# Kernel optimization log

Hardware: AMD Instinct MI355X
Metric: run time of the kernel (lower is better)

## Reference

```python
import jax, jax.numpy as jnp
import numpy as np

N = 4096          # number of leaves
M = 2 * N - 1     # total tree nodes
B = 256           # batch of distribution pairs


def setup_inputs() -> dict:
    key = jax.random.key(0)
    k0, k1, k2, k3, k4, k5 = jax.random.split(key, 6)
    # ancestor-indicator matrix: mostly zeros (structured sparse used densely)
    subtree = (jax.random.uniform(k0, (M, N)) < 0.01).astype(jnp.float32)
    d1 = jax.random.uniform(k1, (N, B), dtype=jnp.float32)
    d2 = jax.random.uniform(k2, (N, B), dtype=jnp.float32)
    ot_distances = jax.random.uniform(k3, (B,), dtype=jnp.float32)
    param = jax.random.normal(k4, (M,), dtype=jnp.float32)
    parents = jax.random.randint(k5, (M,), 0, M, dtype=jnp.int32)
    return {"d1": d1, "d2": d2, "ot_distances": ot_distances,
            "subtree": subtree, "param": param, "parents": parents}


def reference(d1, d2, ot_distances, subtree, param, parents):
    # aggregate leaf mass to every tree node: [M, B]
    m_d1 = jnp.matmul(subtree, d1)
    m_d2 = jnp.matmul(subtree, d2)
    # edge weight = parent height - node height: [M]
    w_v = param[parents] - param
    # tree-Wasserstein-1 per pair: [B]
    w1_tree = 0.5 * jnp.matmul(w_v, jnp.abs(m_d1 - m_d2))
    return jnp.sum(jnp.square(ot_distances - w1_tree))
```

## Files before the change

### kernel.cpp

```cpp
#include <hip/hip_runtime.h>

#define NN    4096
#define MM    8191
#define BB    256
#define HCAP  128

typedef float nfloat4 __attribute__((ext_vector_type(4)));

__device__ __forceinline__ int prefix_lt(unsigned long long m) {
    return __builtin_amdgcn_mbcnt_hi((unsigned)(m >> 32),
           __builtin_amdgcn_mbcnt_lo((unsigned)m, 0u));
}

__device__ __forceinline__ unsigned pack2bf(float lo, float hi) {
    unsigned a = __float_as_uint(lo);
    unsigned b = __float_as_uint(hi);
    a += 0x7fffu + ((a >> 16) & 1u);
    b += 0x7fffu + ((b >> 16) & 1u);
    return (a >> 16) | (b & 0xffff0000u);
}

__global__ __launch_bounds__(256) void k_prep(const float4* __restrict__ d1,
                                              const float4* __restrict__ d2,
                                              float* __restrict__ part2,
                                              uint2* __restrict__ ddp) {
    int idx = blockIdx.x * 256 + threadIdx.x;
    if (idx < 256 * BB) part2[idx] = 0.0f;
    float4 a = d1[idx], b = d2[idx];
    uint2 r;
    r.x = pack2bf(a.x - b.x, a.y - b.y);
    r.y = pack2bf(a.z - b.z, a.w - b.w);
    ddp[idx] = r;
}

__global__ __launch_bounds__(256, 4) void k_fused(
        const nfloat4* __restrict__ st4,
        const uint2* __restrict__ ddp,
        const float* __restrict__ param,
        const int*   __restrict__ parents,
        float* __restrict__ part2) {
    __shared__ unsigned short s_list[2][2][2][HCAP];
    __shared__ int s_cnt[2][2][2];
    __shared__ int s_flag[2][2];
    __shared__ float s_part[BB];
    const int tid  = threadIdx.x;
    const int wave = tid >> 6;
    const int lane = tid & 63;

    s_part[tid] = 0.0f;
    if (tid < 4) s_flag[tid >> 1][tid & 1] = 0;
    __syncthreads();

    const int pipe = wave & 1;
    const int base = blockIdx.x * 2 + pipe;
    float q0 = 0.f, q1 = 0.f, q2 = 0.f, q3 = 0.f;

    if (wave < 2) {
        nfloat4 a0, a1, a2, a3, a4, a5, a6, a7;
        nfloat4 b0, b1, b2, b3, b4, b5, b6, b7;

        #define ISSUE(P, m, h)                                                   \
        {                                                                        \
            const nfloat4* gbase = st4 + (size_t)(m) * (NN / 4) + (h) * (NN / 8);\
            P##0 = __builtin_nontemporal_load(gbase + lane);                     \
            P##1 = __builtin_nontemporal_load(gbase + 64  + lane);               \
            P##2 = __builtin_nontemporal_load(gbase + 128 + lane);               \
            P##3 = __builtin_nontemporal_load(gbase + 192 + lane);               \
            P##4 = __builtin_nontemporal_load(gbase + 256 + lane);               \
            P##5 = __builtin_nontemporal_load(gbase + 320 + lane);               \
            P##6 = __builtin_nontemporal_load(gbase + 384 + lane);               \
            P##7 = __builtin_nontemporal_load(gbase + 448 + lane);               \
        }
        #define SITE(val, col)                                                   \
        {                                                                        \
            unsigned long long mk = __ballot((val) != 0.0f);                     \
            if ((val) != 0.0f)                                                   \
                buf[c + prefix_lt(mk)] = (unsigned short)(col);                  \
            c += __popcll(mk);                                                   \
        }
        #define QUAD(v, cb0)                                                     \
            SITE(v.x, (cb0))     SITE(v.y, (cb0) + 1)                            \
            SITE(v.z, (cb0) + 2) SITE(v.w, (cb0) + 3)
        #define COMPACT(P, h)                                                    \
        {                                                                        \
            const int cb = (h) * (NN / 2);                                       \
            QUAD(P##0, cb + (lane)       * 4)                                    \
            QUAD(P##1, cb + (64  + lane) * 4)                                    \
            QUAD(P##2, cb + (128 + lane) * 4)                                    \
            QUAD(P##3, cb + (192 + lane) * 4)                                    \
            QUAD(P##4, cb + (256 + lane) * 4)                                    \
            QUAD(P##5, cb + (320 + lane) * 4)                                    \
            QUAD(P##6, cb + (384 + lane) * 4)                                    \
            QUAD(P##7, cb + (448 + lane) * 4)                                    \
        }

        if (base < MM) ISSUE(a, base, 0);
        #pragma unroll 1
        for (int i = 0; i < 4; ++i) {
            const int m = base + i * 2048;
            if (m >= MM) break;
            const int slot = i & 1;
            ISSUE(b, m, 1);

            volatile int* f = &s_flag[pipe][slot];
            while (*f != 0) __builtin_amdgcn_s_sleep(2);
            __threadfence_block();

            unsigned short* buf;
            int c;
            buf = s_list[pipe][slot][0]; c = 0;
            COMPACT(a, 0);
            if (lane == 0) s_cnt[pipe][slot][0] = c;

            const int mn = base + (i + 1) * 2048;
            if (mn < MM) ISSUE(a, mn, 0);

            buf = s_list[pipe][slot][1]; c = 0;
            COMPACT(b, 1);
            if (lane == 0) s_cnt[pipe][slot][1] = c;

            __threadfence_block();
            if (lane == 0) *f = i + 1;
        }
        #undef COMPACT
        #undef QUAD
        #undef SITE
        #undef ISSUE
    } else {
        #define UNP0(u) __uint_as_float((u) << 16)
        #define UNP1(u) __uint_as_float((u) & 0xffff0000u)
        #define ACCA(g) { c0 += UNP0(g.x); c1 += UNP1(g.x); c2 += UNP0(g.y); c3 += UNP1(g.y); }
        #define ACCB(g) { e0 += UNP0(g.x); e1 += UNP1(g.x); e2 += UNP0(g.y); e3 += UNP1(g.y); }
        #pragma unroll 1
        for (int i = 0; i < 4; ++i) {
            const int m = base + i * 2048;
            if (m >= MM) break;
            const int slot = i & 1;
            volatile int* f = &s_flag[pipe][slot];
            while (*f != i + 1) __builtin_amdgcn_s_sleep(2);
            __threadfence_block();

            float c0 = 0.f, c1 = 0.f, c2 = 0.f, c3 = 0.f;
            float e0 = 0.f, e1 = 0.f, e2 = 0.f, e3 = 0.f;
            #pragma unroll
            for (int h = 0; h < 2; ++h) {
                const int c = s_cnt[pipe][slot][h];
                const unsigned short* bufr = s_list[pipe][slot][h];
                const unsigned* lw = (const unsigned*)bufr;
                int j = 0;
                for (; j + 8 <= c; j += 8) {
                    unsigned w0 = lw[(j >> 1)    ];
                    unsigned w1 = lw[(j >> 1) + 1];
                    unsigned w2 = lw[(j >> 1) + 2];
                    unsigned w3 = lw[(j >> 1) + 3];
                    unsigned o0 = (w0 & 0xffffu) * 64u + lane;
                    unsigned o1 = (w0 >> 16)     * 64u + lane;
                    unsigned o2 = (w1 & 0xffffu) * 64u + lane;
                    unsigned o3 = (w1 >> 16)     * 64u + lane;
                    unsigned o4 = (w2 & 0xffffu) * 64u + lane;
                    unsigned o5 = (w2 >> 16)     * 64u + lane;
                    unsigned o6 = (w3 & 0xffffu) * 64u + lane;
                    unsigned o7 = (w3 >> 16)     * 64u + lane;
                    uint2 g0 = ddp[o0]; uint2 g1 = ddp[o1];
                    uint2 g2 = ddp[o2]; uint2 g3 = ddp[o3];
                    uint2 g4 = ddp[o4]; uint2 g5 = ddp[o5];
                    uint2 g6 = ddp[o6]; uint2 g7 = ddp[o7];
                    ACCA(g0) ACCB(g1) ACCA(g2) ACCB(g3)
                    ACCA(g4) ACCB(g5) ACCA(g6) ACCB(g7)
                }
                for (; j + 4 <= c; j += 4) {
                    unsigned w0 = lw[(j >> 1)    ];
                    unsigned w1 = lw[(j >> 1) + 1];
                    unsigned o0 = (w0 & 0xffffu) * 64u + lane;
                    unsigned o1 = (w0 >> 16)     * 64u + lane;
                    unsigned o2 = (w1 & 0xffffu) * 64u + lane;
                    unsigned o3 = (w1 >> 16)     * 64u + lane;
                    uint2 g0 = ddp[o0]; uint2 g1 = ddp[o1];
                    uint2 g2 = ddp[o2]; uint2 g3 = ddp[o3];
                    ACCA(g0) ACCB(g1) ACCA(g2) ACCB(g3)
                }
                for (; j < c; ++j) {
                    unsigned n = bufr[j];
                    uint2 g = ddp[n * 64u + lane];
                    ACCA(g)
                }
            }
            __threadfence_block();
            if (lane == 0) *f = 0;

            const float wgt = param[parents[m]] - param[m];
            q0 += wgt * fabsf(c0 + e0);
            q1 += wgt * fabsf(c1 + e1);
            q2 += wgt * fabsf(c2 + e2);
            q3 += wgt * fabsf(c3 + e3);
        }
        #undef ACCA
        #undef ACCB
        #undef UNP0
        #undef UNP1
    }

    atomicAdd(&s_part[4 * lane + 0], q0);
    atomicAdd(&s_part[4 * lane + 1], q1);
    atomicAdd(&s_part[4 * lane + 2], q2);
    atomicAdd(&s_part[4 * lane + 3], q3);
    __syncthreads();
    atomicAdd(&part2[(size_t)(blockIdx.x & 255) * BB + tid], s_part[tid]);
}

__global__ __launch_bounds__(1024) void k_finalize(const float* __restrict__ part2,
                                                   const float* __restrict__ ot,
                                                   float* __restrict__ out) {
    __shared__ float s_red[4][BB];
    __shared__ float s_sq[16];
    const int tid = threadIdx.x;
    const int s = tid >> 8, b = tid & 255;

    float a0 = 0.f, a1 = 0.f, a2 = 0.f, a3 = 0.f;
    float a4 = 0.f, a5 = 0.f, a6 = 0.f, a7 = 0.f;
    #pragma unroll
    for (int j = 0; j < 64; j += 8) {
        int row = s * 64 + j;
        a0 += part2[(row    ) * BB + b];
        a1 += part2[(row + 1) * BB + b];
        a2 += part2[(row + 2) * BB + b];
        a3 += part2[(row + 3) * BB + b];
        a4 += part2[(row + 4) * BB + b];
        a5 += part2[(row + 5) * BB + b];
        a6 += part2[(row + 6) * BB + b];
        a7 += part2[(row + 7) * BB + b];
    }
    s_red[s][b] = ((a0 + a1) + (a2 + a3)) + ((a4 + a5) + (a6 + a7));
    __syncthreads();

    float v = 0.0f;
    if (s == 0) {
        float w1 = (s_red[0][b] + s_red[1][b]) + (s_red[2][b] + s_red[3][b]);
        float e = ot[b] - 0.5f * w1;
        v = e * e;
    }
    #pragma unroll
    for (int off = 32; off > 0; off >>= 1) v += __shfl_down(v, off, 64);
    if ((tid & 63) == 0) s_sq[tid >> 6] = v;
    __syncthreads();
    if (tid == 0) out[0] = (s_sq[0] + s_sq[1]) + (s_sq[2] + s_sq[3]);
}

extern "C" void kernel_launch(void* const* d_in, const int* in_sizes, int n_in,
                              void* d_out, int out_size, void* d_ws, size_t ws_size,
                              hipStream_t stream) {
    const float* d1      = (const float*)d_in[0];
    const float* d2      = (const float*)d_in[1];
    const float* ot      = (const float*)d_in[2];
    const float* subtree = (const float*)d_in[3];
    const float* param   = (const float*)d_in[4];
    const int*   parents = (const int*)d_in[5];

    char* wsb = (char*)d_ws;
    float* part2 = (float*)wsb;
    uint2* ddp   = (uint2*)(wsb + 256 * BB * 4);

    k_prep<<<1024, 256, 0, stream>>>((const float4*)d1, (const float4*)d2,
                                     part2, ddp);
    k_fused<<<1024, 256, 0, stream>>>((const nfloat4*)subtree, ddp,
                                      param, parents, part2);
    k_finalize<<<1, 1024, 0, stream>>>(part2, ot, (float*)d_out);
}
```

Baseline: 51.93 us.

## Widen fused kernel to four producer/consumer pipes per block, dropping register double-buffering

Blocks grow to 512 threads, so each block runs four producer/consumer wave pairs and each pipe handles two rows instead of four. The producer no longer prefetches the next half-row into a second register set; it loads and compacts one half at a time. The intent is to cut register pressure and raise occupancy (launch bounds 512,8), relying on more resident waves rather than in-wave prefetch to hide memory latency. The risk is exposed load latency per wave and a heavier block-level reduction.

```diff
diff --git a/kernel.cpp b/kernel.cpp
--- a/kernel.cpp
+++ b/kernel.cpp
@@ -33,43 +33,41 @@
     ddp[idx] = r;
 }
 
-__global__ __launch_bounds__(256, 4) void k_fused(
+__global__ __launch_bounds__(512, 8) void k_fused(
         const nfloat4* __restrict__ st4,
         const uint2* __restrict__ ddp,
         const float* __restrict__ param,
         const int*   __restrict__ parents,
         float* __restrict__ part2) {
-    __shared__ unsigned short s_list[2][2][2][HCAP];
-    __shared__ int s_cnt[2][2][2];
-    __shared__ int s_flag[2][2];
+    __shared__ unsigned short s_list[4][2][2][HCAP];
+    __shared__ int s_cnt[4][2][2];
+    __shared__ int s_flag[4][2];
     __shared__ float s_part[BB];
     const int tid  = threadIdx.x;
     const int wave = tid >> 6;
     const int lane = tid & 63;
 
-    s_part[tid] = 0.0f;
-    if (tid < 4) s_flag[tid >> 1][tid & 1] = 0;
-    __syncthreads();
-
-    const int pipe = wave & 1;
-    const int base = blockIdx.x * 2 + pipe;
+    if (tid < BB) s_part[tid] = 0.0f;
+    if (tid < 8) s_flag[tid >> 1][tid & 1] = 0;
+    __syncthreads();
+
+    const int pipe = wave & 3;
+    const int pg   = blockIdx.x * 4 + pipe;
     float q0 = 0.f, q1 = 0.f, q2 = 0.f, q3 = 0.f;
 
-    if (wave < 2) {
+    if (wave < 4) {
         nfloat4 a0, a1, a2, a3, a4, a5, a6, a7;
-        nfloat4 b0, b1, b2, b3, b4, b5, b6, b7;
-
-        #define ISSUE(P, m, h)                                                   \
+        #define ISSUE(m, h)                                                      \
         {                                                                        \
-            const nfloat4* gbase = st4 + (size_t)(m) * (NN / 4) + (h) * (NN / 8);\
-            P##0 = __builtin_nontemporal_load(gbase + lane);                     \
-            P##1 = __builtin_nontemporal_load(gbase + 64  + lane);               \
-            P##2 = __builtin_nontemporal_load(gbase + 128 + lane);               \
-            P##3 = __builtin_nontemporal_load(gbase + 192 + lane);               \
-            P##4 = __builtin_nontemporal_load(gbase + 256 + lane);               \
-            P##5 = __builtin_nontemporal_load(gbase + 320 + lane);               \
-            P##6 = __builtin_nontemporal_load(gbase + 384 + lane);               \
-            P##7 = __builtin_nontemporal_load(gbase + 448 + lane);               \
+            const nfloat4* gb = st4 + (size_t)(m) * (NN / 4) + (h) * (NN / 8);   \
+            a0 = __builtin_nontemporal_load(gb + lane);                          \
+            a1 = __builtin_nontemporal_load(gb + 64  + lane);                    \
+            a2 = __builtin_nontemporal_load(gb + 128 + lane);                    \
+            a3 = __builtin_nontemporal_load(gb + 192 + lane);                    \
+            a4 = __builtin_nontemporal_load(gb + 256 + lane);                    \
+            a5 = __builtin_nontemporal_load(gb + 320 + lane);                    \
+            a6 = __builtin_nontemporal_load(gb + 384 + lane);                    \
+            a7 = __builtin_nontemporal_load(gb + 448 + lane);                    \
         }
         #define SITE(val, col)                                                   \
         {                                                                        \
@@ -81,46 +79,42 @@
         #define QUAD(v, cb0)                                                     \
             SITE(v.x, (cb0))     SITE(v.y, (cb0) + 1)                            \
             SITE(v.z, (cb0) + 2) SITE(v.w, (cb0) + 3)
-        #define COMPACT(P, h)                                                    \
+        #define COMPACT(h)                                                       \
         {                                                                        \
             const int cb = (h) * (NN / 2);                                       \
-            QUAD(P##0, cb + (lane)       * 4)                                    \
-            QUAD(P##1, cb + (64  + lane) * 4)                                    \
-            QUAD(P##2, cb + (128 + lane) * 4)                                    \
-            QUAD(P##3, cb + (192 + lane) * 4)                                    \
-            QUAD(P##4, cb + (256 + lane) * 4)                                    \
-            QUAD(P##5, cb + (320 + lane) * 4)                                    \
-            QUAD(P##6, cb + (384 + lane) * 4)                                    \
-            QUAD(P##7, cb + (448 + lane) * 4)                                    \
-        }
-
-        if (base < MM) ISSUE(a, base, 0);
+            QUAD(a0, cb + (lane)       * 4)                                      \
+            QUAD(a1, cb + (64  + lane) * 4)                                      \
+            QUAD(a2, cb + (128 + lane) * 4)                                      \
+            QUAD(a3, cb + (192 + lane) * 4)                                      \
+            QUAD(a4, cb + (256 + lane) * 4)                                      \
+            QUAD(a5, cb + (320 + lane) * 4)                                      \
+            QUAD(a6, cb + (384 + lane) * 4)                                      \
+            QUAD(a7, cb + (448 + lane) * 4)                                      \
+        }
         #pragma unroll 1
-        for (int i = 0; i < 4; ++i) {
-            const int m = base + i * 2048;
+        for (int k = 0; k < 2; ++k) {
+            const int m = pg + k * 4096;
             if (m >= MM) break;
-            const int slot = i & 1;
-            ISSUE(b, m, 1);
-
+            const int slot = k & 1;
             volatile int* f = &s_flag[pipe][slot];
+
+            ISSUE(m, 0);
             while (*f != 0) __builtin_amdgcn_s_sleep(2);
             __threadfence_block();
 
-            unsigned short* buf;
-            int c;
-            buf = s_list[pipe][slot][0]; c = 0;
-            COMPACT(a, 0);
+            unsigned short* buf = s_list[pipe][slot][0];
+            int c = 0;
+            COMPACT(0);
             if (lane == 0) s_cnt[pipe][slot][0] = c;
 
-            const int mn = base + (i + 1) * 2048;
-            if (mn < MM) ISSUE(a, mn, 0);
-
-            buf = s_list[pipe][slot][1]; c = 0;
-            COMPACT(b, 1);
+            ISSUE(m, 1);
+            buf = s_list[pipe][slot][1];
+            c = 0;
+            COMPACT(1);
             if (lane == 0) s_cnt[pipe][slot][1] = c;
 
             __threadfence_block();
-            if (lane == 0) *f = i + 1;
+            if (lane == 0) *f = k + 1;
         }
         #undef COMPACT
         #undef QUAD
@@ -132,12 +126,12 @@
         #define ACCA(g) { c0 += UNP0(g.x); c1 += UNP1(g.x); c2 += UNP0(g.y); c3 += UNP1(g.y); }
         #define ACCB(g) { e0 += UNP0(g.x); e1 += UNP1(g.x); e2 += UNP0(g.y); e3 += UNP1(g.y); }
         #pragma unroll 1
-        for (int i = 0; i < 4; ++i) {
-            const int m = base + i * 2048;
+        for (int k = 0; k < 2; ++k) {
+            const int m = pg + k * 4096;
             if (m >= MM) break;
-            const int slot = i & 1;
+            const int slot = k & 1;
             volatile int* f = &s_flag[pipe][slot];
-            while (*f != i + 1) __builtin_amdgcn_s_sleep(2);
+            while (*f != k + 1) __builtin_amdgcn_s_sleep(2);
             __threadfence_block();
 
             float c0 = 0.f, c1 = 0.f, c2 = 0.f, c3 = 0.f;
@@ -198,14 +192,15 @@
         #undef ACCB
         #undef UNP0
         #undef UNP1
+
+        atomicAdd(&s_part[4 * lane + 0], q0);
+        atomicAdd(&s_part[4 * lane + 1], q1);
+        atomicAdd(&s_part[4 * lane + 2], q2);
+        atomicAdd(&s_part[4 * lane + 3], q3);
     }
-
-    atomicAdd(&s_part[4 * lane + 0], q0);
-    atomicAdd(&s_part[4 * lane + 1], q1);
-    atomicAdd(&s_part[4 * lane + 2], q2);
-    atomicAdd(&s_part[4 * lane + 3], q3);
-    __syncthreads();
-    atomicAdd(&part2[(size_t)(blockIdx.x & 255) * BB + tid], s_part[tid]);
+    __syncthreads();
+    if (tid < BB)
+        atomicAdd(&part2[(size_t)(blockIdx.x & 255) * BB + tid], s_part[tid]);
 }
 
 __global__ __launch_bounds__(1024) void k_finalize(const float* __restrict__ part2,
@@ -262,7 +257,7 @@
 
     k_prep<<<1024, 256, 0, stream>>>((const float4*)d1, (const float4*)d2,
                                      part2, ddp);
-    k_fused<<<1024, 256, 0, stream>>>((const nfloat4*)subtree, ddp,
+    k_fused<<<1024, 512, 0, stream>>>((const nfloat4*)subtree, ddp,
                                       param, parents, part2);
     k_finalize<<<1, 1024, 0, stream>>>(part2, ot, (float*)d_out);
 }
```

New measurement: 50.43 us. -2.9%, faster.
